# Kernel optimization log

Measured on AMD Instinct MI355X. Metric: run time of the kernel, lower is better.

The kernel has to match this reference:

```python
import jax, jax.numpy as jnp
import numpy as np

N, M, C, CSKIP, K = 16384, 4096, 256, 128, 3
BIG = 1e10  # distance penalty for cross-batch pairs


def setup_inputs() -> dict:
    key = jax.random.key(0)
    ks = jax.random.split(key, 6)
    return {
        "x": jax.random.normal(ks[0], (M, C), jnp.float32),
        "pos": jax.random.normal(ks[1], (M, 3), jnp.float32),
        "batch": jnp.zeros((M,), jnp.int32),
        "x_skip": jax.random.normal(ks[2], (N, CSKIP), jnp.float32),
        "pos_skip": jax.random.normal(ks[3], (N, 3), jnp.float32),
        "batch_skip": jnp.zeros((N,), jnp.int32),
        "W1": jax.random.normal(ks[4], (C + CSKIP, 256), jnp.float32) * (1.0 / np.sqrt(C + CSKIP)),
        "b1": jnp.zeros((256,), jnp.float32),
        "W2": jax.random.normal(ks[5], (256, 256), jnp.float32) * (1.0 / np.sqrt(256)),
        "b2": jnp.zeros((256,), jnp.float32),
    }


def _knn_idx(pos, pos_skip, batch, batch_skip, k):
    # Squared distances via GEMM form: [N, M]
    a2 = jnp.sum(pos_skip * pos_skip, axis=-1, keepdims=True)      # [N,1]
    b2 = jnp.sum(pos * pos, axis=-1)[None, :]                       # [1,M]
    d2 = a2 + b2 - 2.0 * (pos_skip @ pos.T)                         # [N,M]
    d2 = jnp.where(batch_skip[:, None] != batch[None, :], BIG, d2)
    _, idx = jax.lax.top_k(-d2, k)                                  # [N,k]
    return idx


def reference(x, pos, batch, x_skip, pos_skip, batch_skip, W1, b1, W2, b2):
    idx = _knn_idx(pos, pos_skip, batch, batch_skip, K)             # [N,k] coarse neighbor ids
    # Exact squared dist recomputed from gathered positions (matches torch diff path)
    diff = pos_skip[:, None, :] - pos[idx]                          # [N,k,3]
    d2 = jnp.sum(diff * diff, axis=-1, keepdims=True)               # [N,k,1]
    w = 1.0 / (d2 + 1e-8)                                           # inverse-distance weights
    wsum = jnp.sum(w, axis=1, keepdims=True)                        # per-row scatter_add == sum over k
    w = w / (wsum + 1e-8)
    x_interp = jnp.sum(w * x[idx], axis=1)                          # [N,C]
    h = jnp.concatenate([x_interp, x_skip], axis=1)                 # [N,C+C']
    h = jax.nn.relu(h @ W1 + b1)
    h = jax.nn.relu(h @ W2 + b2)
    return h
```

## Files before the change

### kernel.cpp

```cpp
#include <hip/hip_runtime.h>

typedef float     f4   __attribute__((ext_vector_type(4)));
typedef float     f32x4 __attribute__((ext_vector_type(4)));
typedef _Float16  h8   __attribute__((ext_vector_type(8)));
typedef _Float16  h4   __attribute__((ext_vector_type(4)));
typedef int       i4   __attribute__((ext_vector_type(4)));

#define NQ   16384
#define MP   4096
#define CF   256
#define CSK  128
#define K1   384
#define HID  256
#define QB   16

__global__ __launch_bounds__(256) void knn_kernel(
    const float* __restrict__ pos,
    const float* __restrict__ pos_skip,
    int*   __restrict__ idx_out,
    float* __restrict__ w_out)
{
    __shared__ float          px[MP];
    __shared__ float          py[MP];
    __shared__ float          pz[MP];
    __shared__ unsigned short ci[QB][96];
    __shared__ unsigned short ci2[QB][16][3];

    const int tid = threadIdx.x;

    for (int j = tid; j < MP; j += 256) {
        px[j] = pos[3*j+0];
        py[j] = pos[3*j+1];
        pz[j] = pos[3*j+2];
    }
    __syncthreads();

    const int lane = tid & 63;
    const int wv   = tid >> 6;

    float qx[4], qy[4], qz[4];
    #pragma unroll
    for (int k = 0; k < 4; k++) {
        const int q = blockIdx.x * QB + wv * 4 + k;
        qx[k] = pos_skip[3*q+0];
        qy[k] = pos_skip[3*q+1];
        qz[k] = pos_skip[3*q+2];
    }

    unsigned K0[4], K1v[4], K2[4];
    #pragma unroll
    for (int k = 0; k < 4; k++) { K0[k] = ~0u; K1v[k] = ~0u; K2[k] = ~0u; }

    #define EVAL(PX, PY, PZ, J)                                               \
        _Pragma("unroll")                                                     \
        for (int k = 0; k < 4; k++) {                                         \
            const float dx = qx[k] - (PX), dy = qy[k] - (PY),                 \
                        dz = qz[k] - (PZ);                                    \
            const float dd = fmaf(dx, dx, fmaf(dy, dy, dz * dz));             \
            const unsigned key = (__float_as_uint(dd) & 0xFFFFF000u) | (J);   \
            const unsigned h0 = max(K0[k], key);                              \
            K0[k] = min(K0[k], key);                                          \
            const unsigned n1 = min(K1v[k], h0);                              \
            const unsigned h1 = max(K1v[k], h0);                              \
            K1v[k] = n1;                                                      \
            K2[k] = min(K2[k], h1);                                           \
        }

    float c0x = px[lane],       c1x = px[lane + 64],
          c2x = px[lane + 128], c3x = px[lane + 192];
    float c0y = py[lane],       c1y = py[lane + 64],
          c2y = py[lane + 128], c3y = py[lane + 192];
    float c0z = pz[lane],       c1z = pz[lane + 64],
          c2z = pz[lane + 128], c3z = pz[lane + 192];

    for (int it = 0; it < 64; it += 4) {
        const unsigned jb = it * 64 + lane;
        const float nx0 = px[jb + 256], nx1 = px[jb + 320],
                    nx2 = px[jb + 384], nx3 = px[jb + 448];
        const float ny0 = py[jb + 256], ny1 = py[jb + 320],
                    ny2 = py[jb + 384], ny3 = py[jb + 448];
        const float nz0 = pz[jb + 256], nz1 = pz[jb + 320],
                    nz2 = pz[jb + 384], nz3 = pz[jb + 448];
        EVAL(c0x, c0y, c0z, jb);
        EVAL(c1x, c1y, c1z, jb + 64);
        EVAL(c2x, c2y, c2z, jb + 128);
        EVAL(c3x, c3y, c3z, jb + 192);
        c0x = nx0; c1x = nx1; c2x = nx2; c3x = nx3;
        c0y = ny0; c1y = ny1; c2y = ny2; c3y = ny3;
        c0z = nz0; c1z = nz1; c2z = nz2; c3z = nz3;
    }
    #undef EVAL

    #pragma unroll
    for (int k = 0; k < 4; k++) {
        const unsigned b0 = (unsigned)__builtin_amdgcn_ds_swizzle((int)K0[k],  0x041F);
        const unsigned b1 = (unsigned)__builtin_amdgcn_ds_swizzle((int)K1v[k], 0x041F);
        const unsigned b2 = (unsigned)__builtin_amdgcn_ds_swizzle((int)K2[k],  0x041F);
        const unsigned m0 = min(K0[k], b0);
        const unsigned c1 = max(K0[k], b0);
        const unsigned d0 = min(K1v[k], b1), d1 = max(K1v[k], b1);
        const unsigned m1 = min(c1, d0);
        const unsigned m2 = min(min(max(c1, d0), d1), min(K2[k], b2));
        if (!(lane & 1)) {
            const int q = wv * 4 + k;
            const int pr = lane >> 1;
            ci[q][pr*3+0] = (unsigned short)(m0 & 0xFFFu);
            ci[q][pr*3+1] = (unsigned short)(m1 & 0xFFFu);
            ci[q][pr*3+2] = (unsigned short)(m2 & 0xFFFu);
        }
    }
    __syncthreads();

    {
        const int q    = tid >> 4;
        const int part = tid & 15;
        const int g    = blockIdx.x * QB + q;
        const double qxd = (double)pos_skip[3*g+0];
        const double qyd = (double)pos_skip[3*g+1];
        const double qzd = (double)pos_skip[3*g+2];
        const double a2d = qxd*qxd + qyd*qyd + qzd*qzd;

        double e0 = 1e300, e1 = 1e300, e2 = 1e300;
        int    j0 = 0,     j1 = 0,     j2 = 0;
        #pragma unroll
        for (int c = 0; c < 6; c++) {
            const int j = ci[q][part*6 + c];
            const double pxd = (double)px[j], pyd = (double)py[j],
                         pzd = (double)pz[j];
            const double b2  = pxd*pxd + pyd*pyd + pzd*pzd;
            const double dot = qxd*pxd + qyd*pyd + qzd*pzd;
            const double d   = (a2d + b2) - 2.0 * dot;
            if (d < e2) {
                if (d < e1) {
                    e2 = e1; j2 = j1;
                    if (d < e0) { e1 = e0; j1 = j0; e0 = d; j0 = j; }
                    else        { e1 = d;  j1 = j; }
                } else { e2 = d; j2 = j; }
            }
        }
        ci2[q][part][0] = (unsigned short)j0;
        ci2[q][part][1] = (unsigned short)j1;
        ci2[q][part][2] = (unsigned short)j2;
    }
    __syncthreads();

    if (tid < QB) {
        const int g = blockIdx.x * QB + tid;
        const double qxd = (double)pos_skip[3*g+0];
        const double qyd = (double)pos_skip[3*g+1];
        const double qzd = (double)pos_skip[3*g+2];
        const double a2d = qxd*qxd + qyd*qyd + qzd*qzd;

        double e0 = 1e300, e1 = 1e300, e2 = 1e300;
        int    j0 = 0,     j1 = 0,     j2 = 0;
        for (int p = 0; p < 16; p++) {
            #pragma unroll
            for (int s = 0; s < 3; s++) {
                const int j = ci2[tid][p][s];
                const double pxd = (double)px[j], pyd = (double)py[j],
                             pzd = (double)pz[j];
                const double b2  = pxd*pxd + pyd*pyd + pzd*pzd;
                const double dot = qxd*pxd + qyd*pyd + qzd*pzd;
                const double d   = (a2d + b2) - 2.0 * dot;
                if (d < e2) {
                    if (d < e1) {
                        e2 = e1; j2 = j1;
                        if (d < e0) { e1 = e0; j1 = j0; e0 = d; j0 = j; }
                        else        { e1 = d;  j1 = j; }
                    } else { e2 = d; j2 = j; }
                }
            }
        }
        const float sx = pos_skip[3*g+0], sy = pos_skip[3*g+1], sz = pos_skip[3*g+2];
        const int jj[3] = { j0, j1, j2 };
        float wv3[3];
        #pragma unroll
        for (int k = 0; k < 3; k++) {
            const float dx = sx - px[jj[k]], dy = sy - py[jj[k]],
                        dz = sz - pz[jj[k]];
            const float dd = dx*dx + dy*dy + dz*dz;
            wv3[k] = 1.0f / (dd + 1e-8f);
        }
        const float inv = 1.0f / (wv3[0] + wv3[1] + wv3[2] + 1e-8f);
        #pragma unroll
        for (int k = 0; k < 3; k++) {
            idx_out[g*3+k] = jj[k];
            w_out[g*3+k]   = wv3[k] * inv;
        }
    }
}

__global__ __launch_bounds__(256) void wconv_kernel(
    const float* __restrict__ W1, const float* __restrict__ W2,
    _Float16* __restrict__ Wt1, _Float16* __restrict__ Wt2)
{
    const int i = blockIdx.x * 256 + threadIdx.x;
    if (i < K1 * HID) {
        const int k = i >> 8, n = i & 255;
        Wt1[(size_t)(k >> 5) * 8192 + ((k >> 3) & 3) * 2048 + n * 8 + (k & 7)]
            = (_Float16)W1[i];
    } else {
        const int i2 = i - K1 * HID;
        const int k = i2 >> 8, n = i2 & 255;
        Wt2[(size_t)(k >> 5) * 8192 + ((k >> 3) & 3) * 2048 + n * 8 + (k & 7)]
            = (_Float16)W2[i2];
    }
}

__global__ __launch_bounds__(256) void mlp_kernel(
    const float* __restrict__ x,
    const float* __restrict__ x_skip,
    const _Float16* __restrict__ Wt1,
    const _Float16* __restrict__ Wt2,
    const float* __restrict__ b1,
    const float* __restrict__ b2,
    const int*   __restrict__ nidx,
    const float* __restrict__ nw,
    float* __restrict__ out)
{
    __shared__ _Float16 As[32][392];
    __shared__ _Float16 Ws[2][8192];
    _Float16 (*Hs)[264] = reinterpret_cast<_Float16 (*)[264]>(&As[0][0]);

    const int tid  = threadIdx.x;
    const int row0 = blockIdx.x * 32;

    {
        const int r   = tid >> 3;
        const int sub = tid & 7;
        const int g   = row0 + r;
        const int j0 = nidx[g*3+0], j1 = nidx[g*3+1], j2 = nidx[g*3+2];
        const float w0 = nw[g*3+0], w1 = nw[g*3+1], w2 = nw[g*3+2];
        const f4* xa = (const f4*)(x + (size_t)j0 * CF);
        const f4* xb = (const f4*)(x + (size_t)j1 * CF);
        const f4* xc = (const f4*)(x + (size_t)j2 * CF);
        const f4* xs = (const f4*)(x_skip + (size_t)g * CSK);
        #pragma unroll
        for (int t = 0; t < 8; t++) {
            const int c4 = t * 8 + sub;
            const f4 a = xa[c4], b = xb[c4], c = xc[c4];
            const f4 v = a * w0 + b * w1 + c * w2;
            h4 hv; hv[0]=(_Float16)v[0]; hv[1]=(_Float16)v[1];
                   hv[2]=(_Float16)v[2]; hv[3]=(_Float16)v[3];
            *(h4*)&As[r][c4 * 4] = hv;
        }
        #pragma unroll
        for (int t = 0; t < 4; t++) {
            const int c4 = t * 8 + sub;
            const f4 v = xs[c4];
            h4 hv; hv[0]=(_Float16)v[0]; hv[1]=(_Float16)v[1];
                   hv[2]=(_Float16)v[2]; hv[3]=(_Float16)v[3];
            *(h4*)&As[r][CF + c4 * 4] = hv;
        }
    }

    const int ln   = tid & 15;
    const int quad = (tid >> 4) & 3;
    const int wv_  = tid >> 6;
    const int nb   = wv_ * 64;
    const int q8   = quad * 8;

    f32x4 acc[2][4];
    #pragma unroll
    for (int mt = 0; mt < 2; mt++)
        #pragma unroll
        for (int nt = 0; nt < 4; nt++) acc[mt][nt] = (f32x4)0.0f;

    i4 R[4];
    #pragma unroll
    for (int t = 0; t < 4; t++)
        R[t] = *(const i4*)(Wt1 + (tid + 256*t) * 8);
    #pragma unroll
    for (int t = 0; t < 4; t++)
        *(i4*)&Ws[0][(tid + 256*t) * 8] = R[t];
    #pragma unroll
    for (int t = 0; t < 4; t++)
        R[t] = *(const i4*)(Wt1 + (size_t)1 * 8192 + (tid + 256*t) * 8);
    __syncthreads();

    for (int kb = 0; kb < 12; kb++) {
        const int buf = kb & 1;
        h8 ha[2], hb[4];
        #pragma unroll
        for (int mt = 0; mt < 2; mt++)
            ha[mt] = *(const h8*)&As[mt*16 + ln][kb*32 + q8];
        #pragma unroll
        for (int nt = 0; nt < 4; nt++)
            hb[nt] = *(const h8*)&Ws[buf][quad * 2048 + (nb + nt*16 + ln) * 8];
        if (kb < 11) {
            #pragma unroll
            for (int t = 0; t < 4; t++)
                *(i4*)&Ws[buf ^ 1][(tid + 256*t) * 8] = R[t];
            const _Float16* src = (kb < 10) ? (Wt1 + (size_t)(kb+2) * 8192)
                                            : Wt2;
            #pragma unroll
            for (int t = 0; t < 4; t++)
                R[t] = *(const i4*)(src + (tid + 256*t) * 8);
        }
        #pragma unroll
        for (int mt = 0; mt < 2; mt++)
            #pragma unroll
            for (int nt = 0; nt < 4; nt++)
                acc[mt][nt] = __builtin_amdgcn_mfma_f32_16x16x32_f16(
                    ha[mt], hb[nt], acc[mt][nt], 0, 0, 0);
        __syncthreads();
    }

    #pragma unroll
    for (int t = 0; t < 4; t++)
        *(i4*)&Ws[0][(tid + 256*t) * 8] = R[t];
    #pragma unroll
    for (int t = 0; t < 4; t++)
        R[t] = *(const i4*)(Wt2 + (size_t)1 * 8192 + (tid + 256*t) * 8);
    #pragma unroll
    for (int nt = 0; nt < 4; nt++) {
        const int n = nb + nt*16 + ln;
        const float bv = b1[n];
        #pragma unroll
        for (int mt = 0; mt < 2; mt++) {
            #pragma unroll
            for (int r = 0; r < 4; r++) {
                const int m = mt*16 + quad*4 + r;
                Hs[m][n] = (_Float16)fmaxf(acc[mt][nt][r] + bv, 0.0f);
            }
            acc[mt][nt] = (f32x4)0.0f;
        }
    }
    __syncthreads();

    for (int kb = 0; kb < 8; kb++) {
        const int buf = kb & 1;
        h8 ha[2], hb[4];
        #pragma unroll
        for (int mt = 0; mt < 2; mt++)
            ha[mt] = *(const h8*)&Hs[mt*16 + ln][kb*32 + q8];
        #pragma unroll
        for (int nt = 0; nt < 4; nt++)
            hb[nt] = *(const h8*)&Ws[buf][quad * 2048 + (nb + nt*16 + ln) * 8];
        if (kb < 7) {
            #pragma unroll
            for (int t = 0; t < 4; t++)
                *(i4*)&Ws[buf ^ 1][(tid + 256*t) * 8] = R[t];
            if (kb < 6) {
                #pragma unroll
                for (int t = 0; t < 4; t++)
                    R[t] = *(const i4*)(Wt2 + (size_t)(kb+2) * 8192 + (tid + 256*t) * 8);
            }
        }
        #pragma unroll
        for (int mt = 0; mt < 2; mt++)
            #pragma unroll
            for (int nt = 0; nt < 4; nt++)
                acc[mt][nt] = __builtin_amdgcn_mfma_f32_16x16x32_f16(
                    ha[mt], hb[nt], acc[mt][nt], 0, 0, 0);
        if (kb < 7) __syncthreads();
    }

    #pragma unroll
    for (int nt = 0; nt < 4; nt++) {
        const int n = nb + nt*16 + ln;
        const float bv = b2[n];
        #pragma unroll
        for (int mt = 0; mt < 2; mt++)
            #pragma unroll
            for (int r = 0; r < 4; r++) {
                const int m = mt*16 + quad*4 + r;
                out[(size_t)(row0 + m) * HID + n] = fmaxf(acc[mt][nt][r] + bv, 0.0f);
            }
    }
}

extern "C" void kernel_launch(void* const* d_in, const int* in_sizes, int n_in,
                              void* d_out, int out_size, void* d_ws, size_t ws_size,
                              hipStream_t stream) {
    const float* x         = (const float*)d_in[0];
    const float* pos       = (const float*)d_in[1];
    const float* x_skip    = (const float*)d_in[3];
    const float* pos_skip  = (const float*)d_in[4];
    const float* W1        = (const float*)d_in[6];
    const float* b1        = (const float*)d_in[7];
    const float* W2        = (const float*)d_in[8];
    const float* b2        = (const float*)d_in[9];
    float* out = (float*)d_out;

    char* ws = (char*)d_ws;
    int*      nidx = (int*)ws;
    float*    nw   = (float*)(ws + 196608);
    _Float16* Wt1  = (_Float16*)(ws + 393216);
    _Float16* Wt2  = (_Float16*)(ws + 589824);

    wconv_kernel<<<(K1*HID + HID*HID) / 256, 256, 0, stream>>>(W1, W2, Wt1, Wt2);
    knn_kernel<<<NQ / QB, 256, 0, stream>>>(pos, pos_skip, nidx, nw);
    mlp_kernel<<<NQ / 32, 256, 0, stream>>>(x, x_skip, Wt1, Wt2, b1, b2, nidx, nw, out);
}
```

Before: 131.4 us.

## Load MLP weight fragments directly from global into registers, drop LDS staging

```diff
diff --git a/kernel.cpp b/kernel.cpp
--- a/kernel.cpp
+++ b/kernel.cpp
@@ -219,7 +219,6 @@
     float* __restrict__ out)
 {
     __shared__ _Float16 As[32][392];
-    __shared__ _Float16 Ws[2][8192];
     _Float16 (*Hs)[264] = reinterpret_cast<_Float16 (*)[264]>(&As[0][0]);
 
     const int tid  = threadIdx.x;
@@ -260,42 +259,42 @@
     const int nb   = wv_ * 64;
     const int q8   = quad * 8;
 
+    const _Float16* w1b = Wt1 + quad * 2048 + (size_t)(nb + ln) * 8;
+    const _Float16* w2b = Wt2 + quad * 2048 + (size_t)(nb + ln) * 8;
+
     f32x4 acc[2][4];
     #pragma unroll
     for (int mt = 0; mt < 2; mt++)
         #pragma unroll
         for (int nt = 0; nt < 4; nt++) acc[mt][nt] = (f32x4)0.0f;
 
-    i4 R[4];
-    #pragma unroll
-    for (int t = 0; t < 4; t++)
-        R[t] = *(const i4*)(Wt1 + (tid + 256*t) * 8);
-    #pragma unroll
-    for (int t = 0; t < 4; t++)
-        *(i4*)&Ws[0][(tid + 256*t) * 8] = R[t];
-    #pragma unroll
-    for (int t = 0; t < 4; t++)
-        R[t] = *(const i4*)(Wt1 + (size_t)1 * 8192 + (tid + 256*t) * 8);
-    __syncthreads();
-
+    h8 B[3][4];
+    #pragma unroll
+    for (int s = 0; s < 3; s++)
+        #pragma unroll
+        for (int nt = 0; nt < 4; nt++)
+            B[s][nt] = *(const h8*)(w1b + (size_t)s * 8192 + nt * 128);
+
+    __syncthreads();
+
+    #pragma unroll
     for (int kb = 0; kb < 12; kb++) {
-        const int buf = kb & 1;
-        h8 ha[2], hb[4];
+        const int s = kb % 3;
+        h8 ha[2];
         #pragma unroll
         for (int mt = 0; mt < 2; mt++)
             ha[mt] = *(const h8*)&As[mt*16 + ln][kb*32 + q8];
-        #pragma unroll
-        for (int nt = 0; nt < 4; nt++)
-            hb[nt] = *(const h8*)&Ws[buf][quad * 2048 + (nb + nt*16 + ln) * 8];
-        if (kb < 11) {
-            #pragma unroll
-            for (int t = 0; t < 4; t++)
-                *(i4*)&Ws[buf ^ 1][(tid + 256*t) * 8] = R[t];
-            const _Float16* src = (kb < 10) ? (Wt1 + (size_t)(kb+2) * 8192)
-                                            : Wt2;
-            #pragma unroll
-            for (int t = 0; t < 4; t++)
-                R[t] = *(const i4*)(src + (tid + 256*t) * 8);
+        h8 hb[4];
+        #pragma unroll
+        for (int nt = 0; nt < 4; nt++) hb[nt] = B[s][nt];
+        if (kb < 9) {
+            #pragma unroll
+            for (int nt = 0; nt < 4; nt++)
+                B[s][nt] = *(const h8*)(w1b + (size_t)(kb+3) * 8192 + nt * 128);
+        } else {
+            #pragma unroll
+            for (int nt = 0; nt < 4; nt++)
+                B[s][nt] = *(const h8*)(w2b + (size_t)(kb-9) * 8192 + nt * 128);
         }
         #pragma unroll
         for (int mt = 0; mt < 2; mt++)
@@ -303,15 +302,9 @@
             for (int nt = 0; nt < 4; nt++)
                 acc[mt][nt] = __builtin_amdgcn_mfma_f32_16x16x32_f16(
                     ha[mt], hb[nt], acc[mt][nt], 0, 0, 0);
-        __syncthreads();
-    }
-
-    #pragma unroll
-    for (int t = 0; t < 4; t++)
-        *(i4*)&Ws[0][(tid + 256*t) * 8] = R[t];
-    #pragma unroll
-    for (int t = 0; t < 4; t++)
-        R[t] = *(const i4*)(Wt2 + (size_t)1 * 8192 + (tid + 256*t) * 8);
+    }
+    __syncthreads();
+
     #pragma unroll
     for (int nt = 0; nt < 4; nt++) {
         const int n = nb + nt*16 + ln;
@@ -328,24 +321,20 @@
     }
     __syncthreads();
 
+    #pragma unroll
     for (int kb = 0; kb < 8; kb++) {
-        const int buf = kb & 1;
-        h8 ha[2], hb[4];
+        const int s = kb % 3;
+        h8 ha[2];
         #pragma unroll
         for (int mt = 0; mt < 2; mt++)
             ha[mt] = *(const h8*)&Hs[mt*16 + ln][kb*32 + q8];
-        #pragma unroll
-        for (int nt = 0; nt < 4; nt++)
-            hb[nt] = *(const h8*)&Ws[buf][quad * 2048 + (nb + nt*16 + ln) * 8];
-        if (kb < 7) {
-            #pragma unroll
-            for (int t = 0; t < 4; t++)
-                *(i4*)&Ws[buf ^ 1][(tid + 256*t) * 8] = R[t];
-            if (kb < 6) {
-                #pragma unroll
-                for (int t = 0; t < 4; t++)
-                    R[t] = *(const i4*)(Wt2 + (size_t)(kb+2) * 8192 + (tid + 256*t) * 8);
-            }
+        h8 hb[4];
+        #pragma unroll
+        for (int nt = 0; nt < 4; nt++) hb[nt] = B[s][nt];
+        if (kb < 5) {
+            #pragma unroll
+            for (int nt = 0; nt < 4; nt++)
+                B[s][nt] = *(const h8*)(w2b + (size_t)(kb+3) * 8192 + nt * 128);
         }
         #pragma unroll
         for (int mt = 0; mt < 2; mt++)
@@ -353,7 +342,6 @@
             for (int nt = 0; nt < 4; nt++)
                 acc[mt][nt] = __builtin_amdgcn_mfma_f32_16x16x32_f16(
                     ha[mt], hb[nt], acc[mt][nt], 0, 0, 0);
-        if (kb < 7) __syncthreads();
     }
 
     #pragma unroll
```

New measurement: 129.7 us. Within noise of the previous version (-1.3%).
